# Kernel tuning notes

Measured on AMD Instinct MI355X. Metric: run time of the kernel, lower is better.

Reference implementation:

```python
import jax, jax.numpy as jnp
import numpy as np


def setup_inputs() -> dict:
    key = jax.random.key(0)
    k1, k2, k3, k4 = jax.random.split(key, 4)
    B, h, w, z, C = 4, 16, 16, 16, 128
    Cq = C // 8
    x = jax.random.normal(k1, (B, h, w, z, C), dtype=jnp.float32)
    # 1x1x1 Conv3D kernels == per-voxel linear projections (he_normal scale)
    Wb = jax.random.normal(k2, (C, Cq), dtype=jnp.float32) * np.sqrt(2.0 / C)
    Wc = jax.random.normal(k3, (C, Cq), dtype=jnp.float32) * np.sqrt(2.0 / C)
    Wd = jax.random.normal(k4, (C, C), dtype=jnp.float32) * np.sqrt(2.0 / C)
    gamma = jnp.zeros((1,), dtype=jnp.float32)
    return {"x": x, "Wb": Wb, "Wc": Wc, "Wd": Wd, "gamma": gamma}


def reference(x, Wb, Wc, Wd, gamma):
    B, h, w, z, C = x.shape
    N = h * w * z
    # 1x1x1 convs = channel projections
    b = jnp.einsum('bhwzc,cf->bhwzf', x, Wb).reshape(B, N, -1)   # [B,N,C/8]
    c = jnp.einsum('bhwzc,cf->bhwzf', x, Wc).reshape(B, N, -1)   # [B,N,C/8]
    d = jnp.einsum('bhwzc,cf->bhwzf', x, Wd).reshape(B, N, C)    # [B,N,C]
    # full NxN attention scores, softmax over last axis (keras softmax default)
    scores = jnp.einsum('bnf,bmf->bnm', b, c)                    # [B,N,N]
    attn = jax.nn.softmax(scores, axis=-1)
    out = jnp.einsum('bnm,bmc->bnc', attn, d).reshape(B, h, w, z, C)
    return gamma * out + x
```

## Files before the change

kernel.cpp:

```cpp
#include <hip/hip_runtime.h>

#define NB     4
#define NN     4096
#define NC     128
#define NCQ    16
#define NROWS  (NB * NN)
#define NSLICE 4
#define NIT    (NN / 64 / NSLICE)

typedef __attribute__((ext_vector_type(8)))  __bf16 bf16x8;
typedef __attribute__((ext_vector_type(4)))  float  f32x4;
typedef __attribute__((ext_vector_type(16))) float  f32x16;

#define MFMA16(a,b,c) __builtin_amdgcn_mfma_f32_16x16x32_bf16((a),(b),(c),0,0,0)
#define MFMA32(a,b,c) __builtin_amdgcn_mfma_f32_32x32x16_bf16((a),(b),(c),0,0,0)
#define LOG2E 1.44269504f

__device__ __forceinline__ f32x16 zero16() {
    f32x16 v;
    #pragma unroll
    for (int i = 0; i < 16; ++i) v[i] = 0.f;
    return v;
}


__global__ void wtrans_kernel(const float* __restrict__ Wb,
                              const float* __restrict__ Wc,
                              const float* __restrict__ Wd,
                              __bf16* __restrict__ wtg)
{
    int oc = blockIdx.x;
    int ch = threadIdx.x;
    float v;
    if      (oc < 16) v = Wb[ch * 16  + oc];
    else if (oc < 32) v = Wc[ch * 16  + (oc - 16)];
    else              v = Wd[ch * 128 + (oc - 32)];
    wtg[oc * 128 + ch] = (__bf16)v;
}

__global__ __launch_bounds__(256) void proj_kernel(
    const float* __restrict__ x, const __bf16* __restrict__ wtg,
    __bf16* __restrict__ qswz, __bf16* __restrict__ kswz, __bf16* __restrict__ vswz)
{
    __shared__ __align__(16) __bf16 xsh[32 * 136];
    __shared__ __align__(16) __bf16 wt [160 * 136];
    __shared__ __align__(16) float  osb[4][16 * 17];

    const int  t    = threadIdx.x;
    const int  lane = t & 63, w = t >> 6;
    const int  q16  = lane & 15, quad = lane >> 4;
    const long row0 = (long)blockIdx.x * 32;
    const int  batch = (int)(row0 >> 12);
    const int  nloc  = (int)(row0 & 4095);
    const int  rh   = w & 1;
    const int  og   = (w >> 1) * 5;

    #pragma unroll
    for (int i = 0; i < 4; ++i) {
        int idx = t + 256 * i;
        int r = idx >> 5, c4 = (idx & 31) * 4;
        float4 xv = *(const float4*)&x[(row0 + r) * NC + c4];
        union { __bf16 h[4]; uint2 u; } cv;
        cv.h[0] = (__bf16)xv.x; cv.h[1] = (__bf16)xv.y;
        cv.h[2] = (__bf16)xv.z; cv.h[3] = (__bf16)xv.w;
        *(uint2*)&xsh[r * 136 + c4] = cv.u;
    }
    #pragma unroll
    for (int i = 0; i < 10; ++i) {
        int idx = t + 256 * i;
        int oc = idx >> 4, seg = idx & 15;
        *(uint4*)&wt[oc * 136 + seg * 8] = ((const uint4*)wtg)[idx];
    }
    __syncthreads();

    bf16x8 xf[4];
    #pragma unroll
    for (int kc = 0; kc < 4; ++kc)
        xf[kc] = *(const bf16x8*)&xsh[(rh * 16 + q16) * 136 + kc * 32 + quad * 8];

    float* osw = osb[w];
    #pragma unroll
    for (int oc_t = 0; oc_t < 5; ++oc_t) {
        const int oset = og + oc_t;
        f32x4 acc = {0.f, 0.f, 0.f, 0.f};
        #pragma unroll
        for (int kc = 0; kc < 4; ++kc) {
            bf16x8 wf = *(const bf16x8*)&wt[(oset * 16 + q16) * 136 + kc * 32 + quad * 8];
            acc = MFMA16(wf, xf[kc], acc);
        }
        #pragma unroll
        for (int r = 0; r < 4; ++r)
            osw[(quad * 4 + r) * 17 + q16] = acc[r];

        if (oset >= 2) {
            int ch_l = lane & 15, lh_t = (lane >> 4) & 1, jh = lane >> 5;
            union { __bf16 h[4]; uint2 u; } cv;
            #pragma unroll
            for (int u2 = 0; u2 < 4; ++u2)
                cv.h[u2] = (__bf16)osw[ch_l * 17 + 8 * jh + 4 * lh_t + u2];
            int kb16 = (nloc >> 4) + rh;
            int cg   = (oset - 2) >> 1;
            int l31v = ((oset - 2) & 1) * 16 + ch_l;
            size_t off = ((((size_t)batch * 256 + kb16) * 4 + cg) << 9)
                       + (size_t)(lh_t * 32 + l31v) * 8 + jh * 4;
            *(uint2*)&vswz[off] = cv.u;
        } else if (lane < 32) {
            int xr = lane & 15, lh_t = lane >> 4;
            const float qsc = (oset == 0) ? LOG2E : 1.f;
            union { __bf16 h[8]; uint4 u; } cv;
            #pragma unroll
            for (int j = 0; j < 8; ++j)
                cv.h[j] = (__bf16)(osw[(8 * lh_t + j) * 17 + xr] * qsc);
            size_t off = ((((size_t)batch * 128 + (nloc >> 5)) * 64)
                       + (size_t)(lh_t * 32 + rh * 16 + xr)) * 8;
            __bf16* dst = (oset == 0) ? qswz : kswz;
            *(uint4*)&dst[off] = cv.u;
        }
    }
}

__global__ __launch_bounds__(256, 3) void attn_kernel(
    const __bf16* __restrict__ qswz, const __bf16* __restrict__ kswz,
    const __bf16* __restrict__ vswz, __bf16* __restrict__ Opart,
    float* __restrict__ lws)
{
    const int t    = threadIdx.x;
    const int lane = t & 63, w = t >> 6;
    const int l31 = lane & 31, lh = lane >> 5;
    const int bid   = blockIdx.x;
    const int xcd   = bid & 7;
    const int batch = xcd >> 1;
    const int sp    = xcd & 1;
    const int qb32  = bid >> 3;
    const int h     = w & 1;
    const int slice = sp * 2 + (w >> 1);
    const int ks0   = slice * (64 * NIT);

    const bf16x8 qf = *(const bf16x8*)
        &qswz[(((size_t)batch * 128 + qb32) * 64 + lane) * 8];

    const __bf16* kptr = kswz + ((size_t)batch * 128 + (ks0 >> 5)) * 512 + lane * 8;
    const __bf16* vptr = vswz + ((size_t)batch * 256 + (ks0 >> 4)) * 2048
                       + h * 1024 + lane * 8;

    f32x16 O0 = zero16(), O1 = zero16();
    float la = 0.f, lb = 0.f;

    bf16x8 kf0 = *(const bf16x8*)(kptr);
    bf16x8 kf1 = *(const bf16x8*)(kptr + 512);
    bf16x8 va[8], vb[8];
    #pragma unroll
    for (int b = 0; b < 4; ++b) {
        va[2*b]     = *(const bf16x8*)(vptr + (size_t)(b * 4)     * 512);
        va[2*b + 1] = *(const bf16x8*)(vptr + (size_t)(b * 4 + 1) * 512);
    }
    f32x16 S0 = MFMA32(kf0, qf, zero16());
    f32x16 S1 = MFMA32(kf1, qf, zero16());

#define ATTN_BODY(IT, CUR, NXT)                                               \
    {                                                                         \
        const int itn = ((IT) + 1 < NIT) ? (IT) + 1 : (IT);                   \
        kf0 = *(const bf16x8*)(kptr + (size_t)itn * 1024);                    \
        kf1 = *(const bf16x8*)(kptr + (size_t)itn * 1024 + 512);              \
        _Pragma("unroll")                                                     \
        for (int b = 0; b < 4; ++b) {                                         \
            NXT[2*b]     = *(const bf16x8*)(vptr + (size_t)((itn*4+b)*4)*512);\
            NXT[2*b + 1] = *(const bf16x8*)(vptr + (size_t)((itn*4+b)*4+1)*512);\
        }                                                                     \
        union { uint32_t u32[16]; bf16x8 f[4]; } pk;                          \
        _Pragma("unroll")                                                     \
        for (int i = 0; i < 8; ++i) {                                         \
            float p0 = __builtin_exp2f(S0[2*i]);                              \
            float p1 = __builtin_exp2f(S0[2*i+1]);                            \
            float p2 = __builtin_exp2f(S1[2*i]);                              \
            float p3 = __builtin_exp2f(S1[2*i+1]);                            \
            la += p0 + p1;                                                    \
            lb += p2 + p3;                                                    \
            uint32_t u0 = __builtin_bit_cast(uint32_t, p0);                   \
            uint32_t u1 = __builtin_bit_cast(uint32_t, p1);                   \
            uint32_t u2 = __builtin_bit_cast(uint32_t, p2);                   \
            uint32_t u3 = __builtin_bit_cast(uint32_t, p3);                   \
            pk.u32[i]     = (u1 & 0xFFFF0000u) | (u0 >> 16);                  \
            pk.u32[8 + i] = (u3 & 0xFFFF0000u) | (u2 >> 16);                  \
        }                                                                     \
        _Pragma("unroll")                                                     \
        for (int b = 0; b < 4; ++b) {                                         \
            O0 = MFMA32(pk.f[b], CUR[2*b],     O0);                           \
            O1 = MFMA32(pk.f[b], CUR[2*b + 1], O1);                           \
        }                                                                     \
        S0 = MFMA32(kf0, qf, zero16());                                       \
        S1 = MFMA32(kf1, qf, zero16());                                       \
    }

    for (int it = 0; it < NIT; it += 2) {
        ATTN_BODY(it,     va, vb);
        ATTN_BODY(it + 1, vb, va);
    }
#undef ATTN_BODY

    float l_tot = la + lb;
    l_tot += __shfl_xor(l_tot, 32);
    const long base = (long)batch * NN;
    if (h == 0 && lane < 32)
        lws[(size_t)slice * NROWS + base + qb32 * 32 + lane] = l_tot;

    #pragma unroll
    for (int ct = 0; ct < 2; ++ct) {
        f32x16 Ov = ct ? O1 : O0;
        #pragma unroll
        for (int r = 0; r < 16; ++r) {
            int q = qb32 * 32 + (r & 3) + 8 * (r >> 2) + 4 * lh;
            Opart[((size_t)slice * NROWS + base + q) * NC + 64 * h + 32 * ct + l31]
                = (__bf16)Ov[r];
        }
    }
}

__global__ __launch_bounds__(256) void combine_kernel(
    const __bf16* __restrict__ Op, const float* __restrict__ lws,
    const float* __restrict__ x, const float* __restrict__ gamma,
    float* __restrict__ out)
{
    __shared__ float gl[32];
    const int  t    = threadIdx.x;
    const long row0 = (long)blockIdx.x * 32;
    if (t < 32) {
        float l = 0.f;
        #pragma unroll
        for (int s = 0; s < NSLICE; ++s) l += lws[(size_t)s * NROWS + row0 + t];
        gl[t] = gamma[0] / l;
    }
    __syncthreads();
    const size_t s1 = (size_t)NROWS * NC;
    #pragma unroll
    for (int i = 0; i < 4; ++i) {
        int idx = t + 256 * i;
        int r = idx >> 5, c4 = (idx & 31) * 4;
        size_t g = (size_t)(row0 + r) * NC + c4;
        float a0 = 0.f, a1 = 0.f, a2 = 0.f, a3 = 0.f;
        #pragma unroll
        for (int s = 0; s < NSLICE; ++s) {
            union { __bf16 h[4]; uint2 u; } a;
            a.u = *(const uint2*)&Op[s1 * s + g];
            a0 += (float)a.h[0]; a1 += (float)a.h[1];
            a2 += (float)a.h[2]; a3 += (float)a.h[3];
        }
        float sc = gl[r];
        float4 xv = *(const float4*)&x[g];
        float4 o;
        o.x = a0 * sc + xv.x; o.y = a1 * sc + xv.y;
        o.z = a2 * sc + xv.z; o.w = a3 * sc + xv.w;
        *(float4*)&out[g] = o;
    }
}

extern "C" void kernel_launch(void* const* d_in, const int* in_sizes, int n_in,
                              void* d_out, int out_size, void* d_ws, size_t ws_size,
                              hipStream_t stream) {
    const float* x     = (const float*)d_in[0];
    const float* Wb    = (const float*)d_in[1];
    const float* Wc    = (const float*)d_in[2];
    const float* Wd    = (const float*)d_in[3];
    const float* gamma = (const float*)d_in[4];
    float*       out   = (float*)d_out;

    __bf16* qswz  = (__bf16*)d_ws;
    __bf16* kswz  = qswz + (size_t)NROWS * NCQ;
    __bf16* vswz  = kswz + (size_t)NROWS * NCQ;
    __bf16* wtg   = vswz + (size_t)NB * NC * NN;
    __bf16* Opart = wtg + 160 * 128;
    float*  lws   = (float*)(Opart + (size_t)NSLICE * NROWS * NC);

    wtrans_kernel <<<160, 128, 0, stream>>>(Wb, Wc, Wd, wtg);
    proj_kernel   <<<NROWS / 32, 256, 0, stream>>>(x, wtg, qswz, kswz, vswz);
    attn_kernel   <<<NB * 128 * 2, 256, 0, stream>>>(qswz, kswz, vswz, Opart, lws);
    combine_kernel<<<NROWS / 32, 256, 0, stream>>>(Opart, lws, x, gamma, out);
}
```

Before: 127.0 us.

## Process two query tiles per wave in attention to reuse K/V fragments

Each attention wave now computes scores and outputs for two 32-row query blocks, sharing each loaded K and V fragment across both. The grid is halved and launch bounds are lowered to two blocks per CU to fit the doubled accumulators. This cuts global K/V traffic per FLOP but reduces occupancy and available parallelism for hiding exp and load latency.

```diff
diff --git a/kernel.cpp b/kernel.cpp
--- a/kernel.cpp
+++ b/kernel.cpp
@@ -119,7 +119,7 @@
     }
 }
 
-__global__ __launch_bounds__(256, 3) void attn_kernel(
+__global__ __launch_bounds__(256, 2) void attn_kernel(
     const __bf16* __restrict__ qswz, const __bf16* __restrict__ kswz,
     const __bf16* __restrict__ vswz, __bf16* __restrict__ Opart,
     float* __restrict__ lws)
@@ -131,20 +131,23 @@
     const int xcd   = bid & 7;
     const int batch = xcd >> 1;
     const int sp    = xcd & 1;
-    const int qb32  = bid >> 3;
+    const int qb64  = bid >> 3;
     const int h     = w & 1;
     const int slice = sp * 2 + (w >> 1);
     const int ks0   = slice * (64 * NIT);
-
-    const bf16x8 qf = *(const bf16x8*)
-        &qswz[(((size_t)batch * 128 + qb32) * 64 + lane) * 8];
+    const int qb32a = qb64 * 2, qb32b = qb64 * 2 + 1;
+
+    const bf16x8 qf0 = *(const bf16x8*)
+        &qswz[(((size_t)batch * 128 + qb32a) * 64 + lane) * 8];
+    const bf16x8 qf1 = *(const bf16x8*)
+        &qswz[(((size_t)batch * 128 + qb32b) * 64 + lane) * 8];
 
     const __bf16* kptr = kswz + ((size_t)batch * 128 + (ks0 >> 5)) * 512 + lane * 8;
     const __bf16* vptr = vswz + ((size_t)batch * 256 + (ks0 >> 4)) * 2048
                        + h * 1024 + lane * 8;
 
-    f32x16 O0 = zero16(), O1 = zero16();
-    float la = 0.f, lb = 0.f;
+    f32x16 O00 = zero16(), O01 = zero16(), O10 = zero16(), O11 = zero16();
+    float l0 = 0.f, l1 = 0.f;
 
     bf16x8 kf0 = *(const bf16x8*)(kptr);
     bf16x8 kf1 = *(const bf16x8*)(kptr + 512);
@@ -154,8 +157,10 @@
         va[2*b]     = *(const bf16x8*)(vptr + (size_t)(b * 4)     * 512);
         va[2*b + 1] = *(const bf16x8*)(vptr + (size_t)(b * 4 + 1) * 512);
     }
-    f32x16 S0 = MFMA32(kf0, qf, zero16());
-    f32x16 S1 = MFMA32(kf1, qf, zero16());
+    f32x16 S0 = MFMA32(kf0, qf0, zero16());
+    f32x16 S1 = MFMA32(kf1, qf0, zero16());
+    f32x16 S2 = MFMA32(kf0, qf1, zero16());
+    f32x16 S3 = MFMA32(kf1, qf1, zero16());
 
 #define ATTN_BODY(IT, CUR, NXT)                                               \
     {                                                                         \
@@ -167,29 +172,43 @@
             NXT[2*b]     = *(const bf16x8*)(vptr + (size_t)((itn*4+b)*4)*512);\
             NXT[2*b + 1] = *(const bf16x8*)(vptr + (size_t)((itn*4+b)*4+1)*512);\
         }                                                                     \
-        union { uint32_t u32[16]; bf16x8 f[4]; } pk;                          \
+        union { uint32_t u32[16]; bf16x8 f[4]; } pk0, pk1;                    \
         _Pragma("unroll")                                                     \
         for (int i = 0; i < 8; ++i) {                                         \
-            float p0 = __builtin_exp2f(S0[2*i]);                              \
-            float p1 = __builtin_exp2f(S0[2*i+1]);                            \
-            float p2 = __builtin_exp2f(S1[2*i]);                              \
-            float p3 = __builtin_exp2f(S1[2*i+1]);                            \
-            la += p0 + p1;                                                    \
-            lb += p2 + p3;                                                    \
-            uint32_t u0 = __builtin_bit_cast(uint32_t, p0);                   \
-            uint32_t u1 = __builtin_bit_cast(uint32_t, p1);                   \
-            uint32_t u2 = __builtin_bit_cast(uint32_t, p2);                   \
-            uint32_t u3 = __builtin_bit_cast(uint32_t, p3);                   \
-            pk.u32[i]     = (u1 & 0xFFFF0000u) | (u0 >> 16);                  \
-            pk.u32[8 + i] = (u3 & 0xFFFF0000u) | (u2 >> 16);                  \
+            float a0 = __builtin_exp2f(S0[2*i]);                              \
+            float a1 = __builtin_exp2f(S0[2*i+1]);                            \
+            float a2 = __builtin_exp2f(S1[2*i]);                              \
+            float a3 = __builtin_exp2f(S1[2*i+1]);                            \
+            float b0 = __builtin_exp2f(S2[2*i]);                              \
+            float b1 = __builtin_exp2f(S2[2*i+1]);                            \
+            float b2 = __builtin_exp2f(S3[2*i]);                              \
+            float b3 = __builtin_exp2f(S3[2*i+1]);                            \
+            l0 += (a0 + a1) + (a2 + a3);                                      \
+            l1 += (b0 + b1) + (b2 + b3);                                      \
+            uint32_t ua0 = __builtin_bit_cast(uint32_t, a0);                  \
+            uint32_t ua1 = __builtin_bit_cast(uint32_t, a1);                  \
+            uint32_t ua2 = __builtin_bit_cast(uint32_t, a2);                  \
+            uint32_t ua3 = __builtin_bit_cast(uint32_t, a3);                  \
+            uint32_t ub0 = __builtin_bit_cast(uint32_t, b0);                  \
+            uint32_t ub1 = __builtin_bit_cast(uint32_t, b1);                  \
+            uint32_t ub2 = __builtin_bit_cast(uint32_t, b2);                  \
+            uint32_t ub3 = __builtin_bit_cast(uint32_t, b3);                  \
+            pk0.u32[i]     = (ua1 & 0xFFFF0000u) | (ua0 >> 16);               \
+            pk0.u32[8 + i] = (ua3 & 0xFFFF0000u) | (ua2 >> 16);               \
+            pk1.u32[i]     = (ub1 & 0xFFFF0000u) | (ub0 >> 16);               \
+            pk1.u32[8 + i] = (ub3 & 0xFFFF0000u) | (ub2 >> 16);               \
         }                                                                     \
         _Pragma("unroll")                                                     \
         for (int b = 0; b < 4; ++b) {                                         \
-            O0 = MFMA32(pk.f[b], CUR[2*b],     O0);                           \
-            O1 = MFMA32(pk.f[b], CUR[2*b + 1], O1);                           \
+            O00 = MFMA32(pk0.f[b], CUR[2*b],     O00);                        \
+            O01 = MFMA32(pk0.f[b], CUR[2*b + 1], O01);                        \
+            O10 = MFMA32(pk1.f[b], CUR[2*b],     O10);                        \
+            O11 = MFMA32(pk1.f[b], CUR[2*b + 1], O11);                        \
         }                                                                     \
-        S0 = MFMA32(kf0, qf, zero16());                                       \
-        S1 = MFMA32(kf1, qf, zero16());                                       \
+        S0 = MFMA32(kf0, qf0, zero16());                                      \
+        S1 = MFMA32(kf1, qf0, zero16());                                      \
+        S2 = MFMA32(kf0, qf1, zero16());                                      \
+        S3 = MFMA32(kf1, qf1, zero16());                                      \
     }
 
     for (int it = 0; it < NIT; it += 2) {
@@ -198,20 +217,26 @@
     }
 #undef ATTN_BODY
 
-    float l_tot = la + lb;
-    l_tot += __shfl_xor(l_tot, 32);
+    l0 += __shfl_xor(l0, 32);
+    l1 += __shfl_xor(l1, 32);
     const long base = (long)batch * NN;
-    if (h == 0 && lane < 32)
-        lws[(size_t)slice * NROWS + base + qb32 * 32 + lane] = l_tot;
-
-    #pragma unroll
-    for (int ct = 0; ct < 2; ++ct) {
-        f32x16 Ov = ct ? O1 : O0;
-        #pragma unroll
-        for (int r = 0; r < 16; ++r) {
-            int q = qb32 * 32 + (r & 3) + 8 * (r >> 2) + 4 * lh;
-            Opart[((size_t)slice * NROWS + base + q) * NC + 64 * h + 32 * ct + l31]
-                = (__bf16)Ov[r];
+    if (h == 0 && lane < 32) {
+        lws[(size_t)slice * NROWS + base + qb32a * 32 + lane] = l0;
+        lws[(size_t)slice * NROWS + base + qb32b * 32 + lane] = l1;
+    }
+
+    #pragma unroll
+    for (int qb = 0; qb < 2; ++qb) {
+        const int q0 = (qb ? qb32b : qb32a) * 32;
+        #pragma unroll
+        for (int ct = 0; ct < 2; ++ct) {
+            f32x16 Ov = qb ? (ct ? O11 : O10) : (ct ? O01 : O00);
+            #pragma unroll
+            for (int r = 0; r < 16; ++r) {
+                int q = q0 + (r & 3) + 8 * (r >> 2) + 4 * lh;
+                Opart[((size_t)slice * NROWS + base + q) * NC + 64 * h + 32 * ct + l31]
+                    = (__bf16)Ov[r];
+            }
         }
     }
 }
@@ -273,6 +298,6 @@
 
     wtrans_kernel <<<160, 128, 0, stream>>>(Wb, Wc, Wd, wtg);
     proj_kernel   <<<NROWS / 32, 256, 0, stream>>>(x, wtg, qswz, kswz, vswz);
-    attn_kernel   <<<NB * 128 * 2, 256, 0, stream>>>(qswz, kswz, vswz, Opart, lws);
+    attn_kernel   <<<NB * 64 * 2, 256, 0, stream>>>(qswz, kswz, vswz, Opart, lws);
     combine_kernel<<<NROWS / 32, 256, 0, stream>>>(Opart, lws, x, gamma, out);
 }
```

After: 127.3 us. Within noise of the previous version (+0.2%).
